# Performance work log

Hardware: AMD Instinct MI355X
Metric: run time of the kernel (lower is better)

## Reference

```python
import jax, jax.numpy as jnp
from jax import lax
import numpy as np

B, T, H = 4096, 512, 32


def _rnn_layer(xs, h0, Wih, Whh, bih, bhh):
    # xs: [T, B, in], h0: [B, H]. torch RNN tanh: h_t = tanh(x W_ih^T + b_ih + h W_hh^T + b_hh)
    def step(h, x_t):
        h = jnp.tanh(x_t @ Wih.T + bih + h @ Whh.T + bhh)
        return h, h
    h_last, ys = lax.scan(step, h0, xs)
    return ys, h_last  # ys: [T, B, H]


def setup_inputs() -> dict:
    key = jax.random.key(0)
    ks = jax.random.split(key, 12)
    s = 0.1  # keep tanh out of saturation
    return {
        "x": jax.random.normal(ks[0], (B, T, 1), jnp.float32),
        "h_state": jnp.zeros((2, B, H), jnp.float32),
        "Wih0": jax.random.normal(ks[1], (H, 1), jnp.float32) * s,
        "Whh0": jax.random.normal(ks[2], (H, H), jnp.float32) * s,
        "bih0": jax.random.normal(ks[3], (H,), jnp.float32) * s,
        "bhh0": jax.random.normal(ks[4], (H,), jnp.float32) * s,
        "Wih1": jax.random.normal(ks[5], (H, H), jnp.float32) * s,
        "Whh1": jax.random.normal(ks[6], (H, H), jnp.float32) * s,
        "bih1": jax.random.normal(ks[7], (H,), jnp.float32) * s,
        "bhh1": jax.random.normal(ks[8], (H,), jnp.float32) * s,
        "Wfc": jax.random.normal(ks[9], (1, H), jnp.float32) * s,
        "bfc": jax.random.normal(ks[10], (1,), jnp.float32) * s,
    }


def reference(x, h_state, Wih0, Whh0, bih0, bhh0, Wih1, Whh1, bih1, bhh1, Wfc, bfc):
    xs = jnp.transpose(x, (1, 0, 2))  # time-major [T, B, 1]
    ys0, h0_last = _rnn_layer(xs, h_state[0], Wih0, Whh0, bih0, bhh0)
    ys1, h1_last = _rnn_layer(ys0, h_state[1], Wih1, Whh1, bih1, bhh1)
    last = ys1[-1]                      # [B, H] == r_out[:, -1, :]
    pred = (last @ Wfc.T + bfc)[:, 0]   # Linear(32,1) then squeeze(-1) -> [B]
    h_new = jnp.stack([h0_last, h1_last], axis=0)  # [2, B, H]
    return pred, h_new
```

## Files before the change

kernel.cpp:

```cpp
#include <hip/hip_runtime.h>

#define BB 4096
#define TT 512
#define HH 32

typedef _Float16 half8 __attribute__((ext_vector_type(8)));
typedef _Float16 h2    __attribute__((ext_vector_type(2)));
typedef float    f32x4 __attribute__((ext_vector_type(4)));

#define MFMA16F(a, b, c) __builtin_amdgcn_mfma_f32_16x16x32_f16((a), (b), (c), 0, 0, 0)

union frag_u { half8 h8; h2 p[4]; };

__device__ __forceinline__ h2 pkrtz(float a, float b) {
    auto r = __builtin_amdgcn_cvt_pkrtz(a, b);
    union { decltype(r) i; h2 o; } u;
    u.i = r;
    return u.o;
}

__device__ __forceinline__ h2 tanh_h2(h2 v) {
    const h2 LO = {(_Float16)(-2.75f), (_Float16)(-2.75f)};
    const h2 HI = {(_Float16)(2.75f), (_Float16)(2.75f)};
    const h2 C0 = {(_Float16)(0.9976293f), (_Float16)(0.9976293f)};
    const h2 C1 = {(_Float16)(-0.3098016f), (_Float16)(-0.3098016f)};
    const h2 C2 = {(_Float16)(0.0889744f), (_Float16)(0.0889744f)};
    const h2 C3 = {(_Float16)(-0.0163448f), (_Float16)(-0.0163448f)};
    const h2 C4 = {(_Float16)(0.0016113f), (_Float16)(0.0016113f)};
    const h2 C5 = {(_Float16)(-0.00006405f), (_Float16)(-0.00006405f)};
    v = __builtin_elementwise_min(v, HI);
    v = __builtin_elementwise_max(v, LO);
    h2 u = v * v;
    h2 t = __builtin_elementwise_fma(u, C5, C4);
    t = __builtin_elementwise_fma(u, t, C3);
    t = __builtin_elementwise_fma(u, t, C2);
    t = __builtin_elementwise_fma(u, t, C1);
    t = __builtin_elementwise_fma(u, t, C0);
    return v * t;
}

__global__ __launch_bounds__(64) void rnn2_mfma(
    const float* __restrict__ x,
    const float* __restrict__ hstate,
    const float* __restrict__ Wih0,
    const float* __restrict__ Whh0,
    const float* __restrict__ bih0,
    const float* __restrict__ bhh0,
    const float* __restrict__ Wih1,
    const float* __restrict__ Whh1,
    const float* __restrict__ bih1,
    const float* __restrict__ bhh1,
    const float* __restrict__ Wfc,
    const float* __restrict__ bfc,
    float* __restrict__ out)
{
    const int l = threadIdx.x;
    const int q = l >> 4;
    const int n = l & 15;
    const int b = blockIdx.x * 16 + n;

    const int r0 = 8 * (n >> 2) + (n & 3);
    half8 A0[2], A1i[2], A1h[2];
#pragma unroll
    for (int t = 0; t < 2; ++t) {
        const int row = r0 + 4 * t;
        const float* p0 = Whh0 + row * HH + q * 8;
        const float* p1 = Wih1 + row * HH + q * 8;
        const float* p2 = Whh1 + row * HH + q * 8;
        frag_u f0, f1, f2;
#pragma unroll
        for (int jj = 0; jj < 4; ++jj) {
            f0.p[jj] = h2{(_Float16)p0[2 * jj], (_Float16)p0[2 * jj + 1]};
            f1.p[jj] = h2{(_Float16)p1[2 * jj], (_Float16)p1[2 * jj + 1]};
            f2.p[jj] = h2{(_Float16)p2[2 * jj], (_Float16)p2[2 * jj + 1]};
        }
        A0[t] = f0.h8; A1i[t] = f1.h8; A1h[t] = f2.h8;
    }

    float wxs[8], b0s[8], wfc8[8];
#pragma unroll
    for (int j = 0; j < 8; ++j) {
        const int hh = 8 * q + j;
        wxs[j]  = Wih0[hh];
        b0s[j]  = bih0[hh] + bhh0[hh];
        wfc8[j] = Wfc[hh];
    }
    f32x4 c1t0, c1t1;
#pragma unroll
    for (int r = 0; r < 4; ++r) {
        c1t0[r] = bih1[8 * q + r] + bhh1[8 * q + r];
        c1t1[r] = bih1[8 * q + 4 + r] + bhh1[8 * q + 4 + r];
    }

    frag_u hb0, hb1;
    {
        const float* p0 = hstate + b * HH + 8 * q;
        const float* p1 = hstate + BB * HH + b * HH + 8 * q;
#pragma unroll
        for (int jj = 0; jj < 4; ++jj) {
            hb0.p[jj] = h2{(_Float16)p0[2 * jj], (_Float16)p0[2 * jj + 1]};
            hb1.p[jj] = h2{(_Float16)p1[2 * jj], (_Float16)p1[2 * jj + 1]};
        }
    }

    f32x4 dbp0, dbp1;

    const float4* xp = (const float4*)(x + (size_t)b * TT);
    float4 xc = xp[0];

    {
        f32x4 c00, c01;
#pragma unroll
        for (int r = 0; r < 4; ++r) {
            c00[r] = fmaf(wxs[r], xc.x, b0s[r]);
            c01[r] = fmaf(wxs[4 + r], xc.x, b0s[4 + r]);
        }
        f32x4 d00 = MFMA16F(A0[0], hb0.h8, c00);
        f32x4 d01 = MFMA16F(A0[1], hb0.h8, c01);
        dbp0 = MFMA16F(A1h[0], hb1.h8, c1t0);
        dbp1 = MFMA16F(A1h[1], hb1.h8, c1t1);
        hb0.p[0] = tanh_h2(pkrtz(d00[0], d00[1]));
        hb0.p[1] = tanh_h2(pkrtz(d00[2], d00[3]));
        hb0.p[2] = tanh_h2(pkrtz(d01[0], d01[1]));
        hb0.p[3] = tanh_h2(pkrtz(d01[2], d01[3]));
    }

#define STEP(XT)                                                              \
    {                                                                         \
        f32x4 d10 = MFMA16F(A1i[0], hb0.h8, dbp0);                            \
        f32x4 d11 = MFMA16F(A1i[1], hb0.h8, dbp1);                            \
        f32x4 c00, c01;                                                       \
        _Pragma("unroll")                                                     \
        for (int r = 0; r < 4; ++r) {                                         \
            c00[r] = fmaf(wxs[r], (XT), b0s[r]);                              \
            c01[r] = fmaf(wxs[4 + r], (XT), b0s[4 + r]);                      \
        }                                                                     \
        f32x4 d00 = MFMA16F(A0[0], hb0.h8, c00);                              \
        f32x4 d01 = MFMA16F(A0[1], hb0.h8, c01);                              \
        hb1.p[0] = tanh_h2(pkrtz(d10[0], d10[1]));                            \
        hb1.p[1] = tanh_h2(pkrtz(d10[2], d10[3]));                            \
        hb1.p[2] = tanh_h2(pkrtz(d11[0], d11[1]));                            \
        hb1.p[3] = tanh_h2(pkrtz(d11[2], d11[3]));                            \
        dbp0 = MFMA16F(A1h[0], hb1.h8, c1t0);                                 \
        dbp1 = MFMA16F(A1h[1], hb1.h8, c1t1);                                 \
        hb0.p[0] = tanh_h2(pkrtz(d00[0], d00[1]));                            \
        hb0.p[1] = tanh_h2(pkrtz(d00[2], d00[3]));                            \
        hb0.p[2] = tanh_h2(pkrtz(d01[0], d01[1]));                            \
        hb0.p[3] = tanh_h2(pkrtz(d01[2], d01[3]));                            \
    }

    for (int k = 0; k < TT / 4 - 1; ++k) {
        float4 xn = xp[k + 1];
        STEP(xc.y);
        STEP(xc.z);
        STEP(xc.w);
        STEP(xn.x);
        xc = xn;
    }
    STEP(xc.y);
    STEP(xc.z);
    STEP(xc.w);

    {
        f32x4 d10 = MFMA16F(A1i[0], hb0.h8, dbp0);
        f32x4 d11 = MFMA16F(A1i[1], hb0.h8, dbp1);
        hb1.p[0] = tanh_h2(pkrtz(d10[0], d10[1]));
        hb1.p[1] = tanh_h2(pkrtz(d10[2], d10[3]));
        hb1.p[2] = tanh_h2(pkrtz(d11[0], d11[1]));
        hb1.p[3] = tanh_h2(pkrtz(d11[2], d11[3]));
    }

    float hf0[8], hf1[8];
#pragma unroll
    for (int jj = 0; jj < 4; ++jj) {
        hf0[2 * jj]     = (float)hb0.p[jj].x;
        hf0[2 * jj + 1] = (float)hb0.p[jj].y;
        hf1[2 * jj]     = (float)hb1.p[jj].x;
        hf1[2 * jj + 1] = (float)hb1.p[jj].y;
    }
    float p = 0.f;
#pragma unroll
    for (int j = 0; j < 8; ++j) p = fmaf(wfc8[j], hf1[j], p);
    p += __shfl_xor(p, 16);
    p += __shfl_xor(p, 32);
    if (q == 0) out[b] = p + bfc[0];

#pragma unroll
    for (int j = 0; j < 8; ++j) {
        out[BB + b * HH + 8 * q + j]           = hf0[j];
        out[BB + BB * HH + b * HH + 8 * q + j] = hf1[j];
    }
}

extern "C" void kernel_launch(void* const* d_in, const int* in_sizes, int n_in,
                              void* d_out, int out_size, void* d_ws, size_t ws_size,
                              hipStream_t stream) {
    const float* x      = (const float*)d_in[0];
    const float* hstate = (const float*)d_in[1];
    const float* Wih0   = (const float*)d_in[2];
    const float* Whh0   = (const float*)d_in[3];
    const float* bih0   = (const float*)d_in[4];
    const float* bhh0   = (const float*)d_in[5];
    const float* Wih1   = (const float*)d_in[6];
    const float* Whh1   = (const float*)d_in[7];
    const float* bih1   = (const float*)d_in[8];
    const float* bhh1   = (const float*)d_in[9];
    const float* Wfc    = (const float*)d_in[10];
    const float* bfc    = (const float*)d_in[11];
    float* out = (float*)d_out;

    dim3 grid(BB / 16);
    dim3 block(64);
    hipLaunchKernelGGL(rnn2_mfma, grid, block, 0, stream,
                       x, hstate, Wih0, Whh0, bih0, bhh0,
                       Wih1, Whh1, bih1, bhh1, Wfc, bfc, out);
}
```

Before: 218.8 us.

## Split each RNN batch tile across two wavefronts exchanging hidden state via LDS

Each 16-sample block now runs with two wavefronts. Each wave computes half of the 32 hidden units for both layers with one MFMA per layer instead of two. The halves of the hidden state are written to a double-buffered shared-memory array and re-read after a __syncthreads every timestep. The aim is to shorten the serial per-step dependency chain and double the waves per CU, at the cost of a block barrier and LDS round trip on every one of the 512 steps.

```diff
diff --git a/kernel.cpp b/kernel.cpp
--- a/kernel.cpp
+++ b/kernel.cpp
@@ -5,12 +5,14 @@
 #define HH 32
 
 typedef _Float16 half8 __attribute__((ext_vector_type(8)));
+typedef _Float16 half4 __attribute__((ext_vector_type(4)));
 typedef _Float16 h2    __attribute__((ext_vector_type(2)));
 typedef float    f32x4 __attribute__((ext_vector_type(4)));
 
 #define MFMA16F(a, b, c) __builtin_amdgcn_mfma_f32_16x16x32_f16((a), (b), (c), 0, 0, 0)
 
 union frag_u { half8 h8; h2 p[4]; };
+union h4u   { half4 v;  h2 p[2]; };
 
 __device__ __forceinline__ h2 pkrtz(float a, float b) {
     auto r = __builtin_amdgcn_cvt_pkrtz(a, b);
@@ -39,7 +41,7 @@
     return v * t;
 }
 
-__global__ __launch_bounds__(64) void rnn2_mfma(
+__global__ __launch_bounds__(128) void rnn2_mfma_ms(
     const float* __restrict__ x,
     const float* __restrict__ hstate,
     const float* __restrict__ Wih0,
@@ -54,16 +56,20 @@
     const float* __restrict__ bfc,
     float* __restrict__ out)
 {
-    const int l = threadIdx.x;
+    const int tid = threadIdx.x;
+    const int l = tid & 63;
+    const int wid = __builtin_amdgcn_readfirstlane(tid >> 6);
     const int q = l >> 4;
     const int n = l & 15;
     const int b = blockIdx.x * 16 + n;
+    const bool w0 = (wid == 0);
+
+    __shared__ half8 xb[2][2][64];
 
     const int r0 = 8 * (n >> 2) + (n & 3);
-    half8 A0[2], A1i[2], A1h[2];
-#pragma unroll
-    for (int t = 0; t < 2; ++t) {
-        const int row = r0 + 4 * t;
+    const int row = r0 + 4 * wid;
+    half8 A0w, A1iw, A1hw;
+    {
         const float* p0 = Whh0 + row * HH + q * 8;
         const float* p1 = Wih1 + row * HH + q * 8;
         const float* p2 = Whh1 + row * HH + q * 8;
@@ -74,100 +80,98 @@
             f1.p[jj] = h2{(_Float16)p1[2 * jj], (_Float16)p1[2 * jj + 1]};
             f2.p[jj] = h2{(_Float16)p2[2 * jj], (_Float16)p2[2 * jj + 1]};
         }
-        A0[t] = f0.h8; A1i[t] = f1.h8; A1h[t] = f2.h8;
-    }
-
-    float wxs[8], b0s[8], wfc8[8];
-#pragma unroll
-    for (int j = 0; j < 8; ++j) {
-        const int hh = 8 * q + j;
-        wxs[j]  = Wih0[hh];
-        b0s[j]  = bih0[hh] + bhh0[hh];
-        wfc8[j] = Wfc[hh];
-    }
-    f32x4 c1t0, c1t1;
+        A0w = f0.h8; A1iw = f1.h8; A1hw = f2.h8;
+    }
+
+    float wxs[4], b0s[4], wfc8[8];
+    f32x4 c1tw;
 #pragma unroll
     for (int r = 0; r < 4; ++r) {
-        c1t0[r] = bih1[8 * q + r] + bhh1[8 * q + r];
-        c1t1[r] = bih1[8 * q + 4 + r] + bhh1[8 * q + 4 + r];
-    }
-
-    frag_u hb0, hb1;
-    {
-        const float* p0 = hstate + b * HH + 8 * q;
-        const float* p1 = hstate + BB * HH + b * HH + 8 * q;
+        const int hh = 8 * q + 4 * wid + r;
+        wxs[r]  = Wih0[hh];
+        b0s[r]  = bih0[hh] + bhh0[hh];
+        c1tw[r] = bih1[hh] + bhh1[hh];
+    }
+#pragma unroll
+    for (int j = 0; j < 8; ++j) wfc8[j] = Wfc[8 * q + j];
+
+    frag_u hb0, hb1i;
+    {
+        const float* p0 = hstate + (size_t)b * HH + 8 * q;
+        const float* p1 = hstate + (size_t)BB * HH + (size_t)b * HH + 8 * q;
 #pragma unroll
         for (int jj = 0; jj < 4; ++jj) {
-            hb0.p[jj] = h2{(_Float16)p0[2 * jj], (_Float16)p0[2 * jj + 1]};
-            hb1.p[jj] = h2{(_Float16)p1[2 * jj], (_Float16)p1[2 * jj + 1]};
+            hb0.p[jj]  = h2{(_Float16)p0[2 * jj], (_Float16)p0[2 * jj + 1]};
+            hb1i.p[jj] = h2{(_Float16)p1[2 * jj], (_Float16)p1[2 * jj + 1]};
         }
     }
 
-    f32x4 dbp0, dbp1;
+    f32x4 dbp = MFMA16F(A1hw, hb1i.h8, c1tw);
+
+    half4* wp0s0 = (half4*)((char*)&xb[0][0][l] + 8 * wid);
+    half4* wp0s1 = (half4*)((char*)&xb[0][1][l] + 8 * wid);
+    half4* wp1s0 = (half4*)((char*)&xb[1][0][l] + 8 * wid);
+    half4* wp1s1 = (half4*)((char*)&xb[1][1][l] + 8 * wid);
 
     const float4* xp = (const float4*)(x + (size_t)b * TT);
     float4 xc = xp[0];
 
     {
-        f32x4 c00, c01;
-#pragma unroll
-        for (int r = 0; r < 4; ++r) {
-            c00[r] = fmaf(wxs[r], xc.x, b0s[r]);
-            c01[r] = fmaf(wxs[4 + r], xc.x, b0s[4 + r]);
-        }
-        f32x4 d00 = MFMA16F(A0[0], hb0.h8, c00);
-        f32x4 d01 = MFMA16F(A0[1], hb0.h8, c01);
-        dbp0 = MFMA16F(A1h[0], hb1.h8, c1t0);
-        dbp1 = MFMA16F(A1h[1], hb1.h8, c1t1);
-        hb0.p[0] = tanh_h2(pkrtz(d00[0], d00[1]));
-        hb0.p[1] = tanh_h2(pkrtz(d00[2], d00[3]));
-        hb0.p[2] = tanh_h2(pkrtz(d01[0], d01[1]));
-        hb0.p[3] = tanh_h2(pkrtz(d01[2], d01[3]));
-    }
-
-#define STEP(XT)                                                              \
+        f32x4 c0;
+#pragma unroll
+        for (int r = 0; r < 4; ++r) c0[r] = fmaf(wxs[r], xc.x, b0s[r]);
+        f32x4 d0 = MFMA16F(A0w, hb0.h8, c0);
+        h4u ho;
+        ho.p[0] = tanh_h2(pkrtz(d0[0], d0[1]));
+        ho.p[1] = tanh_h2(pkrtz(d0[2], d0[3]));
+        *wp0s0 = ho.v;
+        __syncthreads();
+        hb0.h8 = xb[0][0][l];
+    }
+
+#define STEPM(XT, SLOT, WP1, WP0)                                             \
     {                                                                         \
-        f32x4 d10 = MFMA16F(A1i[0], hb0.h8, dbp0);                            \
-        f32x4 d11 = MFMA16F(A1i[1], hb0.h8, dbp1);                            \
-        f32x4 c00, c01;                                                       \
+        f32x4 d1 = MFMA16F(A1iw, hb0.h8, dbp);                                \
+        f32x4 c0;                                                             \
         _Pragma("unroll")                                                     \
-        for (int r = 0; r < 4; ++r) {                                         \
-            c00[r] = fmaf(wxs[r], (XT), b0s[r]);                              \
-            c01[r] = fmaf(wxs[4 + r], (XT), b0s[4 + r]);                      \
-        }                                                                     \
-        f32x4 d00 = MFMA16F(A0[0], hb0.h8, c00);                              \
-        f32x4 d01 = MFMA16F(A0[1], hb0.h8, c01);                              \
-        hb1.p[0] = tanh_h2(pkrtz(d10[0], d10[1]));                            \
-        hb1.p[1] = tanh_h2(pkrtz(d10[2], d10[3]));                            \
-        hb1.p[2] = tanh_h2(pkrtz(d11[0], d11[1]));                            \
-        hb1.p[3] = tanh_h2(pkrtz(d11[2], d11[3]));                            \
-        dbp0 = MFMA16F(A1h[0], hb1.h8, c1t0);                                 \
-        dbp1 = MFMA16F(A1h[1], hb1.h8, c1t1);                                 \
-        hb0.p[0] = tanh_h2(pkrtz(d00[0], d00[1]));                            \
-        hb0.p[1] = tanh_h2(pkrtz(d00[2], d00[3]));                            \
-        hb0.p[2] = tanh_h2(pkrtz(d01[0], d01[1]));                            \
-        hb0.p[3] = tanh_h2(pkrtz(d01[2], d01[3]));                            \
+        for (int r = 0; r < 4; ++r) c0[r] = fmaf(wxs[r], (XT), b0s[r]);       \
+        f32x4 d0 = MFMA16F(A0w, hb0.h8, c0);                                  \
+        h4u h1o;                                                              \
+        h1o.p[0] = tanh_h2(pkrtz(d1[0], d1[1]));                              \
+        h1o.p[1] = tanh_h2(pkrtz(d1[2], d1[3]));                              \
+        *(WP1) = h1o.v;                                                       \
+        h4u h0o;                                                              \
+        h0o.p[0] = tanh_h2(pkrtz(d0[0], d0[1]));                              \
+        h0o.p[1] = tanh_h2(pkrtz(d0[2], d0[3]));                              \
+        *(WP0) = h0o.v;                                                       \
+        __syncthreads();                                                      \
+        frag_u h1f;                                                           \
+        h1f.h8 = xb[1][SLOT][l];                                              \
+        hb0.h8 = xb[0][SLOT][l];                                              \
+        dbp = MFMA16F(A1hw, h1f.h8, c1tw);                                    \
     }
 
     for (int k = 0; k < TT / 4 - 1; ++k) {
         float4 xn = xp[k + 1];
-        STEP(xc.y);
-        STEP(xc.z);
-        STEP(xc.w);
-        STEP(xn.x);
+        STEPM(xc.y, 1, wp1s1, wp0s1);
+        STEPM(xc.z, 0, wp1s0, wp0s0);
+        STEPM(xc.w, 1, wp1s1, wp0s1);
+        STEPM(xn.x, 0, wp1s0, wp0s0);
         xc = xn;
     }
-    STEP(xc.y);
-    STEP(xc.z);
-    STEP(xc.w);
-
-    {
-        f32x4 d10 = MFMA16F(A1i[0], hb0.h8, dbp0);
-        f32x4 d11 = MFMA16F(A1i[1], hb0.h8, dbp1);
-        hb1.p[0] = tanh_h2(pkrtz(d10[0], d10[1]));
-        hb1.p[1] = tanh_h2(pkrtz(d10[2], d10[3]));
-        hb1.p[2] = tanh_h2(pkrtz(d11[0], d11[1]));
-        hb1.p[3] = tanh_h2(pkrtz(d11[2], d11[3]));
+    STEPM(xc.y, 1, wp1s1, wp0s1);
+    STEPM(xc.z, 0, wp1s0, wp0s0);
+    STEPM(xc.w, 1, wp1s1, wp0s1);
+
+    frag_u h1fin;
+    {
+        f32x4 d1 = MFMA16F(A1iw, hb0.h8, dbp);
+        h4u h1o;
+        h1o.p[0] = tanh_h2(pkrtz(d1[0], d1[1]));
+        h1o.p[1] = tanh_h2(pkrtz(d1[2], d1[3]));
+        *wp1s0 = h1o.v;
+        __syncthreads();
+        h1fin.h8 = xb[1][0][l];
     }
 
     float hf0[8], hf1[8];
@@ -175,20 +179,23 @@
     for (int jj = 0; jj < 4; ++jj) {
         hf0[2 * jj]     = (float)hb0.p[jj].x;
         hf0[2 * jj + 1] = (float)hb0.p[jj].y;
-        hf1[2 * jj]     = (float)hb1.p[jj].x;
-        hf1[2 * jj + 1] = (float)hb1.p[jj].y;
-    }
-    float p = 0.f;
-#pragma unroll
-    for (int j = 0; j < 8; ++j) p = fmaf(wfc8[j], hf1[j], p);
-    p += __shfl_xor(p, 16);
-    p += __shfl_xor(p, 32);
-    if (q == 0) out[b] = p + bfc[0];
-
-#pragma unroll
-    for (int j = 0; j < 8; ++j) {
-        out[BB + b * HH + 8 * q + j]           = hf0[j];
-        out[BB + BB * HH + b * HH + 8 * q + j] = hf1[j];
+        hf1[2 * jj]     = (float)h1fin.p[jj].x;
+        hf1[2 * jj + 1] = (float)h1fin.p[jj].y;
+    }
+    if (w0) {
+#pragma unroll
+        for (int j = 0; j < 8; ++j)
+            out[BB + (size_t)b * HH + 8 * q + j] = hf0[j];
+    } else {
+        float p = 0.f;
+#pragma unroll
+        for (int j = 0; j < 8; ++j) p = fmaf(wfc8[j], hf1[j], p);
+        p += __shfl_xor(p, 16);
+        p += __shfl_xor(p, 32);
+        if (q == 0) out[b] = p + bfc[0];
+#pragma unroll
+        for (int j = 0; j < 8; ++j)
+            out[BB + (size_t)BB * HH + (size_t)b * HH + 8 * q + j] = hf1[j];
     }
 }
 
@@ -210,8 +217,8 @@
     float* out = (float*)d_out;
 
     dim3 grid(BB / 16);
-    dim3 block(64);
-    hipLaunchKernelGGL(rnn2_mfma, grid, block, 0, stream,
+    dim3 block(128);
+    hipLaunchKernelGGL(rnn2_mfma_ms, grid, block, 0, stream,
                        x, hstate, Wih0, Whh0, bih0, bhh0,
                        Wih1, Whh1, bih1, bhh1, Wfc, bfc, out);
 }
```

Result: faster. 206.6 us (-5.5%).

## Split layer-0 hidden rows across two waves with LDS exchange per step

Applied to the files above, without the earlier changes.

Each block now runs two wavefronts that each compute half of the layer-0 hidden-state MFMA and tanh. The halves are exchanged through double-buffered shared memory with a barrier every timestep. Both waves redundantly compute layer 1, and the output writes are split between them. The aim is to shorten the per-step serial critical path by halving layer-0 work per wave and by doubling the waves in flight. The cost is a block barrier and an LDS round trip on every recurrent step.

```diff
diff --git a/kernel.cpp b/kernel.cpp
--- a/kernel.cpp
+++ b/kernel.cpp
@@ -5,12 +5,14 @@
 #define HH 32
 
 typedef _Float16 half8 __attribute__((ext_vector_type(8)));
+typedef _Float16 half4 __attribute__((ext_vector_type(4)));
 typedef _Float16 h2    __attribute__((ext_vector_type(2)));
 typedef float    f32x4 __attribute__((ext_vector_type(4)));
 
 #define MFMA16F(a, b, c) __builtin_amdgcn_mfma_f32_16x16x32_f16((a), (b), (c), 0, 0, 0)
 
 union frag_u { half8 h8; h2 p[4]; };
+union h4u   { half4 v;  h2 p[2]; };
 
 __device__ __forceinline__ h2 pkrtz(float a, float b) {
     auto r = __builtin_amdgcn_cvt_pkrtz(a, b);
@@ -39,7 +41,14 @@
     return v * t;
 }
 
-__global__ __launch_bounds__(64) void rnn2_mfma(
+#define XBAR()                                                    \
+    do {                                                          \
+        asm volatile("s_waitcnt lgkmcnt(0)" ::: "memory");        \
+        __builtin_amdgcn_s_barrier();                             \
+        asm volatile("" ::: "memory");                            \
+    } while (0)
+
+__global__ __launch_bounds__(128) void rnn2_mfma_hs(
     const float* __restrict__ x,
     const float* __restrict__ hstate,
     const float* __restrict__ Wih0,
@@ -54,36 +63,48 @@
     const float* __restrict__ bfc,
     float* __restrict__ out)
 {
-    const int l = threadIdx.x;
+    const int tid = threadIdx.x;
+    const int l = tid & 63;
+    const int wid = __builtin_amdgcn_readfirstlane(tid >> 6);
     const int q = l >> 4;
     const int n = l & 15;
     const int b = blockIdx.x * 16 + n;
+    const bool w0 = (wid == 0);
+
+    __shared__ half4 xbH[2][2][64];
 
     const int r0 = 8 * (n >> 2) + (n & 3);
-    half8 A0[2], A1i[2], A1h[2];
+    half8 A1i[2], A1h[2];
 #pragma unroll
     for (int t = 0; t < 2; ++t) {
         const int row = r0 + 4 * t;
-        const float* p0 = Whh0 + row * HH + q * 8;
         const float* p1 = Wih1 + row * HH + q * 8;
         const float* p2 = Whh1 + row * HH + q * 8;
-        frag_u f0, f1, f2;
+        frag_u f1, f2;
 #pragma unroll
         for (int jj = 0; jj < 4; ++jj) {
-            f0.p[jj] = h2{(_Float16)p0[2 * jj], (_Float16)p0[2 * jj + 1]};
             f1.p[jj] = h2{(_Float16)p1[2 * jj], (_Float16)p1[2 * jj + 1]};
             f2.p[jj] = h2{(_Float16)p2[2 * jj], (_Float16)p2[2 * jj + 1]};
         }
-        A0[t] = f0.h8; A1i[t] = f1.h8; A1h[t] = f2.h8;
-    }
-
-    float wxs[8], b0s[8], wfc8[8];
-#pragma unroll
-    for (int j = 0; j < 8; ++j) {
-        const int hh = 8 * q + j;
-        wxs[j]  = Wih0[hh];
-        b0s[j]  = bih0[hh] + bhh0[hh];
-        wfc8[j] = Wfc[hh];
+        A1i[t] = f1.h8; A1h[t] = f2.h8;
+    }
+    half8 A0w;
+    {
+        const int row = r0 + 4 * wid;
+        const float* p0 = Whh0 + row * HH + q * 8;
+        frag_u f0;
+#pragma unroll
+        for (int jj = 0; jj < 4; ++jj)
+            f0.p[jj] = h2{(_Float16)p0[2 * jj], (_Float16)p0[2 * jj + 1]};
+        A0w = f0.h8;
+    }
+
+    float wxs[4], b0s[4], wfc8[8];
+#pragma unroll
+    for (int r = 0; r < 4; ++r) {
+        const int hh = 8 * q + 4 * wid + r;
+        wxs[r] = Wih0[hh];
+        b0s[r] = bih0[hh] + bhh0[hh];
     }
     f32x4 c1t0, c1t1;
 #pragma unroll
@@ -91,11 +112,13 @@
         c1t0[r] = bih1[8 * q + r] + bhh1[8 * q + r];
         c1t1[r] = bih1[8 * q + 4 + r] + bhh1[8 * q + 4 + r];
     }
+#pragma unroll
+    for (int j = 0; j < 8; ++j) wfc8[j] = Wfc[8 * q + j];
 
     frag_u hb0, hb1;
     {
-        const float* p0 = hstate + b * HH + 8 * q;
-        const float* p1 = hstate + BB * HH + b * HH + 8 * q;
+        const float* p0 = hstate + (size_t)b * HH + 8 * q;
+        const float* p1 = hstate + (size_t)BB * HH + (size_t)b * HH + 8 * q;
 #pragma unroll
         for (int jj = 0; jj < 4; ++jj) {
             hb0.p[jj] = h2{(_Float16)p0[2 * jj], (_Float16)p0[2 * jj + 1]};
@@ -103,63 +126,66 @@
         }
     }
 
-    f32x4 dbp0, dbp1;
+    f32x4 dbp0 = MFMA16F(A1h[0], hb1.h8, c1t0);
+    f32x4 dbp1 = MFMA16F(A1h[1], hb1.h8, c1t1);
 
     const float4* xp = (const float4*)(x + (size_t)b * TT);
     float4 xc = xp[0];
 
     {
-        f32x4 c00, c01;
-#pragma unroll
-        for (int r = 0; r < 4; ++r) {
-            c00[r] = fmaf(wxs[r], xc.x, b0s[r]);
-            c01[r] = fmaf(wxs[4 + r], xc.x, b0s[4 + r]);
-        }
-        f32x4 d00 = MFMA16F(A0[0], hb0.h8, c00);
-        f32x4 d01 = MFMA16F(A0[1], hb0.h8, c01);
-        dbp0 = MFMA16F(A1h[0], hb1.h8, c1t0);
-        dbp1 = MFMA16F(A1h[1], hb1.h8, c1t1);
-        hb0.p[0] = tanh_h2(pkrtz(d00[0], d00[1]));
-        hb0.p[1] = tanh_h2(pkrtz(d00[2], d00[3]));
-        hb0.p[2] = tanh_h2(pkrtz(d01[0], d01[1]));
-        hb0.p[3] = tanh_h2(pkrtz(d01[2], d01[3]));
-    }
-
-#define STEP(XT)                                                              \
+        f32x4 c0;
+#pragma unroll
+        for (int r = 0; r < 4; ++r) c0[r] = fmaf(wxs[r], xc.x, b0s[r]);
+        f32x4 d0 = MFMA16F(A0w, hb0.h8, c0);
+        h4u ho;
+        ho.p[0] = tanh_h2(pkrtz(d0[0], d0[1]));
+        ho.p[1] = tanh_h2(pkrtz(d0[2], d0[3]));
+        xbH[wid][0][l] = ho.v;
+        XBAR();
+        h4u lo, hi;
+        lo.v = xbH[0][0][l];
+        hi.v = xbH[1][0][l];
+        hb0.p[0] = lo.p[0]; hb0.p[1] = lo.p[1];
+        hb0.p[2] = hi.p[0]; hb0.p[3] = hi.p[1];
+    }
+
+#define STEPB(XT, SLOT)                                                       \
     {                                                                         \
         f32x4 d10 = MFMA16F(A1i[0], hb0.h8, dbp0);                            \
         f32x4 d11 = MFMA16F(A1i[1], hb0.h8, dbp1);                            \
-        f32x4 c00, c01;                                                       \
+        f32x4 c0;                                                             \
         _Pragma("unroll")                                                     \
-        for (int r = 0; r < 4; ++r) {                                         \
-            c00[r] = fmaf(wxs[r], (XT), b0s[r]);                              \
-            c01[r] = fmaf(wxs[4 + r], (XT), b0s[4 + r]);                      \
-        }                                                                     \
-        f32x4 d00 = MFMA16F(A0[0], hb0.h8, c00);                              \
-        f32x4 d01 = MFMA16F(A0[1], hb0.h8, c01);                              \
+        for (int r = 0; r < 4; ++r) c0[r] = fmaf(wxs[r], (XT), b0s[r]);       \
+        f32x4 d0 = MFMA16F(A0w, hb0.h8, c0);                                  \
+        h4u ho;                                                               \
+        ho.p[0] = tanh_h2(pkrtz(d0[0], d0[1]));                               \
+        ho.p[1] = tanh_h2(pkrtz(d0[2], d0[3]));                               \
+        xbH[wid][SLOT][l] = ho.v;                                             \
+        XBAR();                                                               \
+        h4u lo, hi;                                                           \
+        lo.v = xbH[0][SLOT][l];                                               \
+        hi.v = xbH[1][SLOT][l];                                               \
         hb1.p[0] = tanh_h2(pkrtz(d10[0], d10[1]));                            \
         hb1.p[1] = tanh_h2(pkrtz(d10[2], d10[3]));                            \
         hb1.p[2] = tanh_h2(pkrtz(d11[0], d11[1]));                            \
         hb1.p[3] = tanh_h2(pkrtz(d11[2], d11[3]));                            \
         dbp0 = MFMA16F(A1h[0], hb1.h8, c1t0);                                 \
         dbp1 = MFMA16F(A1h[1], hb1.h8, c1t1);                                 \
-        hb0.p[0] = tanh_h2(pkrtz(d00[0], d00[1]));                            \
-        hb0.p[1] = tanh_h2(pkrtz(d00[2], d00[3]));                            \
-        hb0.p[2] = tanh_h2(pkrtz(d01[0], d01[1]));                            \
-        hb0.p[3] = tanh_h2(pkrtz(d01[2], d01[3]));                            \
+        hb0.p[0] = lo.p[0]; hb0.p[1] = lo.p[1];                               \
+        hb0.p[2] = hi.p[0]; hb0.p[3] = hi.p[1];                               \
     }
 
     for (int k = 0; k < TT / 4 - 1; ++k) {
         float4 xn = xp[k + 1];
-        STEP(xc.y);
-        STEP(xc.z);
-        STEP(xc.w);
-        STEP(xn.x);
+        STEPB(xc.y, 1);
+        STEPB(xc.z, 0);
+        STEPB(xc.w, 1);
+        STEPB(xn.x, 0);
         xc = xn;
     }
-    STEP(xc.y);
-    STEP(xc.z);
-    STEP(xc.w);
+    STEPB(xc.y, 1);
+    STEPB(xc.z, 0);
+    STEPB(xc.w, 1);
 
     {
         f32x4 d10 = MFMA16F(A1i[0], hb0.h8, dbp0);
@@ -178,17 +204,20 @@
         hf1[2 * jj]     = (float)hb1.p[jj].x;
         hf1[2 * jj + 1] = (float)hb1.p[jj].y;
     }
-    float p = 0.f;
-#pragma unroll
-    for (int j = 0; j < 8; ++j) p = fmaf(wfc8[j], hf1[j], p);
-    p += __shfl_xor(p, 16);
-    p += __shfl_xor(p, 32);
-    if (q == 0) out[b] = p + bfc[0];
-
-#pragma unroll
-    for (int j = 0; j < 8; ++j) {
-        out[BB + b * HH + 8 * q + j]           = hf0[j];
-        out[BB + BB * HH + b * HH + 8 * q + j] = hf1[j];
+    if (w0) {
+#pragma unroll
+        for (int j = 0; j < 8; ++j)
+            out[BB + (size_t)b * HH + 8 * q + j] = hf0[j];
+    } else {
+        float p = 0.f;
+#pragma unroll
+        for (int j = 0; j < 8; ++j) p = fmaf(wfc8[j], hf1[j], p);
+        p += __shfl_xor(p, 16);
+        p += __shfl_xor(p, 32);
+        if (q == 0) out[b] = p + bfc[0];
+#pragma unroll
+        for (int j = 0; j < 8; ++j)
+            out[BB + (size_t)BB * HH + (size_t)b * HH + 8 * q + j] = hf1[j];
     }
 }
 
@@ -210,8 +239,8 @@
     float* out = (float*)d_out;
 
     dim3 grid(BB / 16);
-    dim3 block(64);
-    hipLaunchKernelGGL(rnn2_mfma, grid, block, 0, stream,
+    dim3 block(128);
+    hipLaunchKernelGGL(rnn2_mfma_hs, grid, block, 0, stream,
                        x, hstate, Wih0, Whh0, bih0, bhh0,
                        Wih1, Whh1, bih1, bhh1, Wfc, bfc, out);
 }
```

Result: faster. 204.6 us (-6.5%).

## Lag layer-1 by two steps so input projection is precomputed off critical path

Applied to the files above, without the earlier changes.

Layer 1 now runs two timesteps behind layer 0 instead of one. Its input projection (Wih1·h0) is computed one step ahead and carried in registers as the accumulator for the recurrent MFMA. The recurrent chain for layer 1 then holds one MFMA pair per step, where before it waited on the Whh1 MFMA feeding the Wih1 MFMA. The cost is an extra prologue and epilogue step and a few more live registers.

```diff
diff --git a/kernel.cpp b/kernel.cpp
--- a/kernel.cpp
+++ b/kernel.cpp
@@ -39,7 +39,7 @@
     return v * t;
 }
 
-__global__ __launch_bounds__(64) void rnn2_mfma(
+__global__ __launch_bounds__(64) void rnn2_mfma_lag2(
     const float* __restrict__ x,
     const float* __restrict__ hstate,
     const float* __restrict__ Wih0,
@@ -94,8 +94,8 @@
 
     frag_u hb0, hb1;
     {
-        const float* p0 = hstate + b * HH + 8 * q;
-        const float* p1 = hstate + BB * HH + b * HH + 8 * q;
+        const float* p0 = hstate + (size_t)b * HH + 8 * q;
+        const float* p1 = hstate + (size_t)BB * HH + (size_t)b * HH + 8 * q;
 #pragma unroll
         for (int jj = 0; jj < 4; ++jj) {
             hb0.p[jj] = h2{(_Float16)p0[2 * jj], (_Float16)p0[2 * jj + 1]};
@@ -103,10 +103,10 @@
         }
     }
 
-    f32x4 dbp0, dbp1;
-
     const float4* xp = (const float4*)(x + (size_t)b * TT);
     float4 xc = xp[0];
+
+    f32x4 e0p, e1p;
 
     {
         f32x4 c00, c01;
@@ -117,18 +117,34 @@
         }
         f32x4 d00 = MFMA16F(A0[0], hb0.h8, c00);
         f32x4 d01 = MFMA16F(A0[1], hb0.h8, c01);
-        dbp0 = MFMA16F(A1h[0], hb1.h8, c1t0);
-        dbp1 = MFMA16F(A1h[1], hb1.h8, c1t1);
         hb0.p[0] = tanh_h2(pkrtz(d00[0], d00[1]));
         hb0.p[1] = tanh_h2(pkrtz(d00[2], d00[3]));
         hb0.p[2] = tanh_h2(pkrtz(d01[0], d01[1]));
         hb0.p[3] = tanh_h2(pkrtz(d01[2], d01[3]));
     }
+    {
+        e0p = MFMA16F(A1i[0], hb0.h8, c1t0);
+        e1p = MFMA16F(A1i[1], hb0.h8, c1t1);
+        f32x4 c00, c01;
+#pragma unroll
+        for (int r = 0; r < 4; ++r) {
+            c00[r] = fmaf(wxs[r], xc.y, b0s[r]);
+            c01[r] = fmaf(wxs[4 + r], xc.y, b0s[4 + r]);
+        }
+        f32x4 d00 = MFMA16F(A0[0], hb0.h8, c00);
+        f32x4 d01 = MFMA16F(A0[1], hb0.h8, c01);
+        hb0.p[0] = tanh_h2(pkrtz(d00[0], d00[1]));
+        hb0.p[1] = tanh_h2(pkrtz(d00[2], d00[3]));
+        hb0.p[2] = tanh_h2(pkrtz(d01[0], d01[1]));
+        hb0.p[3] = tanh_h2(pkrtz(d01[2], d01[3]));
+    }
 
 #define STEP(XT)                                                              \
     {                                                                         \
-        f32x4 d10 = MFMA16F(A1i[0], hb0.h8, dbp0);                            \
-        f32x4 d11 = MFMA16F(A1i[1], hb0.h8, dbp1);                            \
+        f32x4 d10 = MFMA16F(A1h[0], hb1.h8, e0p);                             \
+        f32x4 d11 = MFMA16F(A1h[1], hb1.h8, e1p);                             \
+        f32x4 en0 = MFMA16F(A1i[0], hb0.h8, c1t0);                            \
+        f32x4 en1 = MFMA16F(A1i[1], hb0.h8, c1t1);                            \
         f32x4 c00, c01;                                                       \
         _Pragma("unroll")                                                     \
         for (int r = 0; r < 4; ++r) {                                         \
@@ -141,29 +157,38 @@
         hb1.p[1] = tanh_h2(pkrtz(d10[2], d10[3]));                            \
         hb1.p[2] = tanh_h2(pkrtz(d11[0], d11[1]));                            \
         hb1.p[3] = tanh_h2(pkrtz(d11[2], d11[3]));                            \
-        dbp0 = MFMA16F(A1h[0], hb1.h8, c1t0);                                 \
-        dbp1 = MFMA16F(A1h[1], hb1.h8, c1t1);                                 \
         hb0.p[0] = tanh_h2(pkrtz(d00[0], d00[1]));                            \
         hb0.p[1] = tanh_h2(pkrtz(d00[2], d00[3]));                            \
         hb0.p[2] = tanh_h2(pkrtz(d01[0], d01[1]));                            \
         hb0.p[3] = tanh_h2(pkrtz(d01[2], d01[3]));                            \
+        e0p = en0; e1p = en1;                                                 \
     }
 
     for (int k = 0; k < TT / 4 - 1; ++k) {
         float4 xn = xp[k + 1];
-        STEP(xc.y);
         STEP(xc.z);
         STEP(xc.w);
         STEP(xn.x);
+        STEP(xn.y);
         xc = xn;
     }
-    STEP(xc.y);
     STEP(xc.z);
     STEP(xc.w);
 
     {
-        f32x4 d10 = MFMA16F(A1i[0], hb0.h8, dbp0);
-        f32x4 d11 = MFMA16F(A1i[1], hb0.h8, dbp1);
+        f32x4 d10 = MFMA16F(A1h[0], hb1.h8, e0p);
+        f32x4 d11 = MFMA16F(A1h[1], hb1.h8, e1p);
+        f32x4 en0 = MFMA16F(A1i[0], hb0.h8, c1t0);
+        f32x4 en1 = MFMA16F(A1i[1], hb0.h8, c1t1);
+        hb1.p[0] = tanh_h2(pkrtz(d10[0], d10[1]));
+        hb1.p[1] = tanh_h2(pkrtz(d10[2], d10[3]));
+        hb1.p[2] = tanh_h2(pkrtz(d11[0], d11[1]));
+        hb1.p[3] = tanh_h2(pkrtz(d11[2], d11[3]));
+        e0p = en0; e1p = en1;
+    }
+    {
+        f32x4 d10 = MFMA16F(A1h[0], hb1.h8, e0p);
+        f32x4 d11 = MFMA16F(A1h[1], hb1.h8, e1p);
         hb1.p[0] = tanh_h2(pkrtz(d10[0], d10[1]));
         hb1.p[1] = tanh_h2(pkrtz(d10[2], d10[3]));
         hb1.p[2] = tanh_h2(pkrtz(d11[0], d11[1]));
@@ -187,8 +212,8 @@
 
 #pragma unroll
     for (int j = 0; j < 8; ++j) {
-        out[BB + b * HH + 8 * q + j]           = hf0[j];
-        out[BB + BB * HH + b * HH + 8 * q + j] = hf1[j];
+        out[BB + (size_t)b * HH + 8 * q + j]                  = hf0[j];
+        out[BB + (size_t)BB * HH + (size_t)b * HH + 8 * q + j] = hf1[j];
     }
 }
 
@@ -211,7 +236,7 @@
 
     dim3 grid(BB / 16);
     dim3 block(64);
-    hipLaunchKernelGGL(rnn2_mfma, grid, block, 0, stream,
+    hipLaunchKernelGGL(rnn2_mfma_lag2, grid, block, 0, stream,
                        x, hstate, Wih0, Whh0, bih0, bhh0,
                        Wih1, Whh1, bih1, bhh1, Wfc, bfc, out);
 }
```

Result: faster. 214.1 us (-2.1%).
